# Kernel tuning notes

Measured on AMD Instinct MI355X. Metric: run time of the kernel, lower is better.

## Reference

```python
import jax, jax.numpy as jnp
import numpy as np

EPS = float(np.finfo(np.float64).eps)  # matches np.finfo(float).eps in torch combine()
TOP_K = 2


def setup_inputs() -> dict:
    key = jax.random.key(0)
    k0, k1, k2, k3 = jax.random.split(key, 4)
    N, D, F, E = 8192, 512, 2048, 8
    s = 0.02  # init scale keeps exp() in combine numerically tame
    return {
        "x": jax.random.normal(k0, (N, D), jnp.float32),
        "Wg": jax.random.normal(k1, (D, E), jnp.float32) * s,
        "W1": jax.random.normal(k2, (E, D, F), jnp.float32) * s,
        "b1": jnp.zeros((E, F), jnp.float32),
        "W2": jax.random.normal(k3, (E, F, D), jnp.float32) * s,
        "b2": jnp.zeros((E, D), jnp.float32),
    }


def reference(x, Wg, W1, b1, W2, b2):
    """Sparse-MoE token routing: gate -> dispatch -> per-expert MLP -> combine.

    Faithful to the torch dispatch()/combine() helpers: experts produce
    log-domain outputs; combine() does exp, gate-weighted scatter-add, eps
    floor, then log. Here expressed as dense masked expert compute (zero
    gates annihilate non-routed contributions), which is mathematically
    identical to the gather/index_add formulation and fully vectorized.
    """
    N, D = x.shape
    E = Wg.shape[1]
    # --- gating: noisy-free top-k softmax gates, scattered to [N, E] ---
    logits = x @ Wg                                    # [N, E]
    top_vals, top_idx = jax.lax.top_k(logits, TOP_K)   # [N, K]
    top_gates = jax.nn.softmax(top_vals, axis=-1)      # [N, K]
    gates = jnp.zeros((N, E), x.dtype).at[jnp.arange(N)[:, None], top_idx].set(top_gates)
    # --- expert MLPs (ReLU, per activation='relu' default) ---
    h = jax.nn.relu(jnp.einsum('nd,edf->nef', x, W1) + b1[None])  # [N, E, F]
    o = jnp.einsum('nef,efd->ned', h, W2) + b2[None]              # [N, E, D]
    # --- combine: gate-weighted sum of exp(expert_out), eps floor, log ---
    combined = jnp.einsum('ne,ned->nd', gates, jnp.exp(o))        # [N, D]
    combined = jnp.where(combined == 0, EPS, combined)
    return jnp.log(combined)
```

## Files before the change

### kernel.cpp

```cpp
#include <hip/hip_runtime.h>
#include <stdint.h>
#include <math.h>

#define NTOK 8192
#define DIM  512
#define FDIM 2048
#define NEXP 8
#define RMAX 17408
#define NMT  136
#define KSPLIT 2

typedef __attribute__((ext_vector_type(8))) __bf16 bf16x8;
typedef __attribute__((ext_vector_type(4))) float  f32x4;

#define GTPB 16
#define GB_BLOCKS (NTOK / GTPB)
#define PREP_W1 (GB_BLOCKS)
#define PREP_W2 (GB_BLOCKS + 8192)

#define OFF_W1T    ((size_t)0)
#define SZ_W1T     ((size_t)NEXP * DIM * FDIM * 2)
#define OFF_W2T    (OFF_W1T + SZ_W1T)
#define SZ_W2T     SZ_W1T
#define OFF_H      (OFF_W2T + SZ_W2T)
#define SZ_H       ((size_t)RMAX * FDIM * 2)
#define OFF_META   (OFF_H + SZ_H)
#define SZ_META    ((size_t)1024)
#define OFF_XG     (OFF_META + SZ_META)
#define SZ_XG      ((size_t)RMAX * DIM * 2)
#define OFF_O1     OFF_XG
#define OFF_O0     (OFF_XG + SZ_XG)
#define SZ_O0      ((size_t)RMAX * DIM * 4)
#define OFF_TOKE   (OFF_O0 + SZ_O0)
#define OFF_TOKLS  (OFF_TOKE + (size_t)NTOK * 8)
#define OFF_TOKG   (OFF_TOKLS + (size_t)NTOK * 8)
#define OFF_HISTP  (OFF_TOKG + (size_t)NTOK * 8)
#define OFF_BASEP  (OFF_HISTP + (size_t)GB_BLOCKS * NEXP * 4)
#define OFF_ROWS   (OFF_BASEP + (size_t)GB_BLOCKS * NEXP * 4)

__device__ __forceinline__ unsigned short f2bf(float f) {
  union { float f; unsigned int u; } v; v.f = f;
  unsigned int u = v.u;
  return (unsigned short)((u + 0x7fffu + ((u >> 16) & 1u)) >> 16);
}
__device__ __forceinline__ float bf2f(unsigned short u) {
  union { unsigned int u; float f; } v; v.u = ((unsigned int)u) << 16;
  return v.f;
}

__device__ __forceinline__ void gld16(const unsigned short* g, unsigned short* l) {
  __builtin_amdgcn_global_load_lds(
      (const __attribute__((address_space(1))) void*)g,
      (__attribute__((address_space(3))) void*)l, 16, 0, 0);
}

__device__ __forceinline__ void transpose_tile(const float* __restrict__ src,
                                               unsigned short* __restrict__ dst,
                                               int R, int C, int bx, int by, int bz) {
  __shared__ float t[32][33];
  const int r0 = by * 32, c0 = bx * 32;
  const float* s = src + (size_t)bz * R * C;
  unsigned short* d = dst + (size_t)bz * R * C;
  const int tr = threadIdx.x >> 5, tc = threadIdx.x & 31;
  #pragma unroll
  for (int i = 0; i < 4; i++)
    t[tr + i * 8][tc] = s[(size_t)(r0 + tr + i * 8) * C + (c0 + tc)];
  __syncthreads();
  #pragma unroll
  for (int i = 0; i < 4; i++)
    d[(size_t)(c0 + tr + i * 8) * R + (r0 + tc)] = f2bf(t[tc][tr + i * 8]);
}

__device__ __forceinline__ void gate_body(int gb, const float* __restrict__ x,
                            const float* __restrict__ Wg,
                            int* __restrict__ hist_part, int2* __restrict__ tok_e,
                            int2* __restrict__ tok_ls, float2* __restrict__ tok_g) {
  __shared__ int hist[NEXP];
  __shared__ int le[GTPB][2];
  __shared__ int ls[GTPB][2];
  __shared__ float lg[GTPB][2];
  const int wid = threadIdx.x >> 6;
  const int lane = threadIdx.x & 63;
  if (threadIdx.x < NEXP) hist[threadIdx.x] = 0;
  __syncthreads();
  for (int t = 0; t < 4; t++) {
    const int lt = wid * 4 + t;
    const int n = gb * GTPB + lt;
    double acc[NEXP];
    #pragma unroll
    for (int e = 0; e < NEXP; e++) acc[e] = 0.0;
    #pragma unroll
    for (int i = 0; i < 8; i++) {
      int dd = lane + i * 64;
      double xv = (double)x[(size_t)n * DIM + dd];
      const float* wr = Wg + (size_t)dd * NEXP;
      #pragma unroll
      for (int e = 0; e < NEXP; e++) acc[e] += xv * (double)wr[e];
    }
    #pragma unroll
    for (int s = 32; s > 0; s >>= 1)
      #pragma unroll
      for (int e = 0; e < NEXP; e++) acc[e] += __shfl_xor(acc[e], s, 64);
    if (lane == 0) {
      int i0 = 0;
      #pragma unroll
      for (int e = 1; e < NEXP; e++) if (acc[e] > acc[i0]) i0 = e;
      int i1 = (i0 == 0) ? 1 : 0;
      #pragma unroll
      for (int e = 0; e < NEXP; e++) { if (e == i0 || e == i1) continue; if (acc[e] > acc[i1]) i1 = e; }
      double e1 = exp(acc[i1] - acc[i0]), ssum = 1.0 + e1;
      le[lt][0] = i0; le[lt][1] = i1;
      ls[lt][0] = atomicAdd(&hist[i0], 1);
      ls[lt][1] = atomicAdd(&hist[i1], 1);
      lg[lt][0] = (float)(1.0 / ssum); lg[lt][1] = (float)(e1 / ssum);
    }
  }
  __syncthreads();
  if (threadIdx.x < NEXP) hist_part[gb * NEXP + threadIdx.x] = hist[threadIdx.x];
  if (threadIdx.x < GTPB) {
    const int lt = threadIdx.x;
    const int n = gb * GTPB + lt;
    tok_e[n]  = make_int2(le[lt][0], le[lt][1]);
    tok_ls[n] = make_int2(ls[lt][0], ls[lt][1]);
    tok_g[n]  = make_float2(lg[lt][0], lg[lt][1]);
  }
}

__global__ __launch_bounds__(256) void prep_kernel(const float* __restrict__ W1,
    unsigned short* __restrict__ W1t, const float* __restrict__ W2,
    unsigned short* __restrict__ W2t, const float* __restrict__ x,
    const float* __restrict__ Wg, int* __restrict__ hist_part, int2* __restrict__ tok_e,
    int2* __restrict__ tok_ls, float2* __restrict__ tok_g) {
  const int b = blockIdx.x;
  if (b < GB_BLOCKS) {
    gate_body(b, x, Wg, hist_part, tok_e, tok_ls, tok_g);
  } else if (b < PREP_W2) {
    const int q = b - PREP_W1;
    transpose_tile(W1, W1t, DIM, FDIM, q & 63, (q >> 6) & 15, q >> 10);
  } else {
    const int q = b - PREP_W2;
    transpose_tile(W2, W2t, FDIM, DIM, q & 15, (q >> 4) & 63, q >> 10);
  }
}

__global__ __launch_bounds__(256) void scan_kernel(const int* __restrict__ hist_part,
    int* __restrict__ offsets, int* __restrict__ base_part, int* __restrict__ mtile_e) {
  __shared__ int hp[GB_BLOCKS * NEXP];
  __shared__ int segsum[8][NEXP];
  __shared__ int segbase[8][NEXP];
  __shared__ int tot[NEXP];
  __shared__ int soff[NEXP + 1];
  for (int i = threadIdx.x; i < GB_BLOCKS * NEXP; i += 256) hp[i] = hist_part[i];
  __syncthreads();
  if (threadIdx.x < 64) {
    const int e = threadIdx.x & 7, s = threadIdx.x >> 3;
    int run = 0;
    for (int b = s * 64; b < s * 64 + 64; b++) {
      int v = hp[b * NEXP + e]; hp[b * NEXP + e] = run; run += v;
    }
    segsum[s][e] = run;
  }
  __syncthreads();
  if (threadIdx.x < NEXP) {
    const int e = threadIdx.x;
    int run = 0;
    for (int s = 0; s < 8; s++) { segbase[s][e] = run; run += segsum[s][e]; }
    tot[e] = run;
  }
  __syncthreads();
  if (threadIdx.x == 0) {
    int off = 0;
    for (int e = 0; e < NEXP; e++) { soff[e] = off; offsets[e] = off; off += (tot[e] + 127) & ~127; }
    soff[NEXP] = off; offsets[NEXP] = off;
    for (int t = 0; t < NMT; t++) {
      int r = t * 128, e = NEXP - 1;
      for (int q = 0; q < NEXP; q++)
        if (r >= soff[q] && r < soff[q + 1]) { e = q; break; }
      mtile_e[t] = e;
    }
  }
  __syncthreads();
  for (int i = threadIdx.x; i < GB_BLOCKS * NEXP; i += 256) {
    const int b = i >> 3, e = i & 7;
    base_part[i] = soff[e] + segbase[b >> 6][e] + hp[i];
  }
}

__global__ void gather_kernel(const float* __restrict__ x, const int2* __restrict__ tok_e,
                              const int2* __restrict__ tok_ls, const int* __restrict__ base_part,
                              ushort4* __restrict__ xg, int2* __restrict__ rows) {
  const int n = blockIdx.x;
  int2 te = tok_e[n]; int2 tl = tok_ls[n];
  const int gb = n / GTPB;
  const int r0 = base_part[gb * NEXP + te.x] + tl.x;
  const int r1 = base_part[gb * NEXP + te.y] + tl.y;
  if (threadIdx.x == 0) rows[n] = make_int2(r0, r1);
  const float4* xr = (const float4*)(x + (size_t)n * DIM);
  float4 v = xr[threadIdx.x];
  ushort4 o;
  o.x = f2bf(v.x); o.y = f2bf(v.y); o.z = f2bf(v.z); o.w = f2bf(v.w);
  xg[(size_t)r0 * (DIM / 4) + threadIdx.x] = o;
  xg[(size_t)r1 * (DIM / 4) + threadIdx.x] = o;
}

template <int K, int LDA, int LDB>
__device__ __forceinline__ void gemm_core(const unsigned short* __restrict__ A,
                                          const unsigned short* __restrict__ B,
                                          int m0, int n0, f32x4 acc[4][4]) {
  __shared__ __align__(16) unsigned short As[128 * 64];
  __shared__ __align__(16) unsigned short Bs[128 * 64];
  const int tid = threadIdx.x;
  const int wid = tid >> 6, lane = tid & 63;
  const int wm = (wid >> 1) * 64, wn = (wid & 1) * 64;
  const int quad = lane >> 4, l16 = lane & 15;
  const int srow = tid >> 3;
  const int scol = ((tid & 7) ^ (srow & 7)) << 3;
  unsigned short* As_w = As + 512 * wid;
  unsigned short* Bs_w = Bs + 512 * wid;
  const int r7 = (l16 & 7) << 3;
  const unsigned short* Ar = A + (size_t)(m0 + srow) * LDA + scol;
  const unsigned short* Br = B + (size_t)(n0 + srow) * LDB + scol;
  #pragma unroll 1
  for (int kt = 0; kt < K; kt += 64) {
    __syncthreads();
    #pragma unroll
    for (int p = 0; p < 4; p++) {
      gld16(Ar + (size_t)(32 * p) * LDA + kt, As_w + p * 2048);
      gld16(Br + (size_t)(32 * p) * LDB + kt, Bs_w + p * 2048);
    }
    __syncthreads();
    #pragma unroll
    for (int kk = 0; kk < 2; kk++) {
      const int swz = ((kk * 4 + quad) << 3) ^ r7;
      bf16x8 af[4], bfr[4];
      #pragma unroll
      for (int i = 0; i < 4; i++) {
        af[i]  = *(const bf16x8*)(As + (wm + i * 16 + l16) * 64 + swz);
        bfr[i] = *(const bf16x8*)(Bs + (wn + i * 16 + l16) * 64 + swz);
      }
      #pragma unroll
      for (int mi = 0; mi < 4; mi++)
        #pragma unroll
        for (int ni = 0; ni < 4; ni++)
          acc[mi][ni] = __builtin_amdgcn_mfma_f32_16x16x32_bf16(af[mi], bfr[ni], acc[mi][ni], 0, 0, 0);
    }
  }
}

__global__ __launch_bounds__(256, 4) void gemm1_kernel(const unsigned short* __restrict__ xg,
    const unsigned short* __restrict__ W1t, const int* __restrict__ mtile_e,
    const float* __restrict__ b1, unsigned short* __restrict__ h) {
  const int bm = blockIdx.x, bn = blockIdx.y;
  const int e = mtile_e[bm];
  f32x4 acc[4][4];
  #pragma unroll
  for (int i = 0; i < 4; i++)
    #pragma unroll
    for (int j = 0; j < 4; j++) acc[i][j] = (f32x4){0.f, 0.f, 0.f, 0.f};
  gemm_core<DIM, DIM, DIM>(xg, W1t + (size_t)e * FDIM * DIM, bm * 128, bn * 128, acc);
  const int tid = threadIdx.x, wid = tid >> 6, lane = tid & 63;
  const int wm = (wid >> 1) * 64, wn = (wid & 1) * 64, quad = lane >> 4, l16 = lane & 15;
  #pragma unroll
  for (int mi = 0; mi < 4; mi++) {
    #pragma unroll
    for (int ni = 0; ni < 4; ni++) {
      const int col = bn * 128 + wn + ni * 16 + l16;
      const float bb = b1[e * FDIM + col];
      #pragma unroll
      for (int r = 0; r < 4; r++) {
        const int row = bm * 128 + wm + mi * 16 + quad * 4 + r;
        float v = acc[mi][ni][r] + bb;
        h[(size_t)row * FDIM + col] = f2bf(v > 0.f ? v : 0.f);
      }
    }
  }
}

__global__ __launch_bounds__(256, 4) void gemm2_kernel(const unsigned short* __restrict__ h,
    const unsigned short* __restrict__ W2t, const int* __restrict__ mtile_e,
    float* __restrict__ o0, unsigned short* __restrict__ o1) {
  const int bm = blockIdx.x, bn = blockIdx.y, ks = blockIdx.z;
  const int e = mtile_e[bm];
  const int k0 = ks * (FDIM / KSPLIT);
  f32x4 acc[4][4];
  #pragma unroll
  for (int i = 0; i < 4; i++)
    #pragma unroll
    for (int j = 0; j < 4; j++) acc[i][j] = (f32x4){0.f, 0.f, 0.f, 0.f};
  gemm_core<FDIM / KSPLIT, FDIM, FDIM>(h + k0, W2t + (size_t)e * DIM * FDIM + k0,
                                       bm * 128, bn * 128, acc);
  const int tid = threadIdx.x, wid = tid >> 6, lane = tid & 63;
  const int wm = (wid >> 1) * 64, wn = (wid & 1) * 64, quad = lane >> 4, l16 = lane & 15;
  if (ks == 0) {
    #pragma unroll
    for (int mi = 0; mi < 4; mi++)
      #pragma unroll
      for (int r = 0; r < 4; r++) {
        const int row = bm * 128 + wm + mi * 16 + quad * 4 + r;
        #pragma unroll
        for (int ni = 0; ni < 4; ni++) {
          const int col = bn * 128 + wn + ni * 16 + l16;
          o0[(size_t)row * DIM + col] = acc[mi][ni][r];
        }
      }
  } else {
    #pragma unroll
    for (int mi = 0; mi < 4; mi++)
      #pragma unroll
      for (int r = 0; r < 4; r++) {
        const int row = bm * 128 + wm + mi * 16 + quad * 4 + r;
        #pragma unroll
        for (int ni = 0; ni < 4; ni++) {
          const int col = bn * 128 + wn + ni * 16 + l16;
          o1[(size_t)row * DIM + col] = f2bf(acc[mi][ni][r]);
        }
      }
  }
}

__global__ void combine_kernel(const float* __restrict__ o0, const unsigned short* __restrict__ o1,
                               const int2* __restrict__ tok_e, const int2* __restrict__ rows,
                               const float2* __restrict__ tok_g, const float* __restrict__ b2,
                               float* __restrict__ out) {
  const int n = blockIdx.x;
  const int c = threadIdx.x * 4;
  int2 te = tok_e[n]; int2 rr = rows[n]; float2 tg = tok_g[n];
  const int r0 = rr.x, r1 = rr.y;
  float4 a0 = *(const float4*)(o0 + (size_t)r0 * DIM + c);
  float4 a1 = *(const float4*)(o0 + (size_t)r1 * DIM + c);
  ushort4 p0 = *(const ushort4*)(o1 + (size_t)r0 * DIM + c);
  ushort4 p1 = *(const ushort4*)(o1 + (size_t)r1 * DIM + c);
  float4 c0 = *(const float4*)(b2 + te.x * DIM + c);
  float4 c1 = *(const float4*)(b2 + te.y * DIM + c);
  float4 res;
  #pragma unroll
  for (int j = 0; j < 4; j++) {
    float v0 = ((const float*)&a0)[j] + bf2f(((const unsigned short*)&p0)[j]) + ((const float*)&c0)[j];
    float v1 = ((const float*)&a1)[j] + bf2f(((const unsigned short*)&p1)[j]) + ((const float*)&c1)[j];
    float v = tg.x * expf(v0) + tg.y * expf(v1);
    v = (v == 0.0f) ? 2.220446049250313e-16f : v;
    ((float*)&res)[j] = logf(v);
  }
  *(float4*)(out + (size_t)n * DIM + c) = res;
}

extern "C" void kernel_launch(void* const* d_in, const int* in_sizes, int n_in,
                              void* d_out, int out_size, void* d_ws, size_t ws_size,
                              hipStream_t stream) {
  const float* x  = (const float*)d_in[0];
  const float* Wg = (const float*)d_in[1];
  const float* W1 = (const float*)d_in[2];
  const float* b1 = (const float*)d_in[3];
  const float* W2 = (const float*)d_in[4];
  const float* b2 = (const float*)d_in[5];
  float* out = (float*)d_out;
  char* ws = (char*)d_ws;

  unsigned short* W1t = (unsigned short*)(ws + OFF_W1T);
  unsigned short* W2t = (unsigned short*)(ws + OFF_W2T);
  unsigned short* h   = (unsigned short*)(ws + OFF_H);
  int* meta    = (int*)(ws + OFF_META);
  int* offsets = meta;
  int* mtile_e = meta + 16;
  unsigned short* xg = (unsigned short*)(ws + OFF_XG);
  unsigned short* o1 = (unsigned short*)(ws + OFF_O1);
  float* o0      = (float*)(ws + OFF_O0);
  int2* tok_e    = (int2*)(ws + OFF_TOKE);
  int2* tok_ls   = (int2*)(ws + OFF_TOKLS);
  float2* tok_g  = (float2*)(ws + OFF_TOKG);
  int* hist_part = (int*)(ws + OFF_HISTP);
  int* base_part = (int*)(ws + OFF_BASEP);
  int2* rows     = (int2*)(ws + OFF_ROWS);

  prep_kernel<<<GB_BLOCKS + 2 * 8192, 256, 0, stream>>>(W1, W1t, W2, W2t, x, Wg,
                                                        hist_part, tok_e, tok_ls, tok_g);
  scan_kernel<<<1, 256, 0, stream>>>(hist_part, offsets, base_part, mtile_e);
  gather_kernel<<<NTOK, 128, 0, stream>>>(x, tok_e, tok_ls, base_part, (ushort4*)xg, rows);
  gemm1_kernel<<<dim3(NMT, FDIM / 128), 256, 0, stream>>>(xg, W1t, mtile_e, b1, h);
  gemm2_kernel<<<dim3(NMT, DIM / 128, KSPLIT), 256, 0, stream>>>(h, W2t, mtile_e, o0, o1);
  combine_kernel<<<NTOK, 128, 0, stream>>>(o0, o1, tok_e, rows, tok_g, b2, out);
}
```

Measured before the change: 294.3 us.

## Double-buffer GEMM LDS tiles and use 64x64 weight transpose tiles

The shared GEMM core now keeps two LDS buffers and issues global-to-LDS loads for the next K tile while running MFMAs on the current one, cutting the barrier-separated load/compute stalls to one sync per iteration. Launch bounds drop from 4 to 2 blocks per CU to fit the doubled shared memory. Separately, the weight transpose in the prep kernel moves from 32x32 to 64x64 tiles, launching four times fewer blocks with more work each. The risk is lower occupancy hiding less latency and a larger LDS footprint in the prep kernel.

```diff
diff --git a/kernel.cpp b/kernel.cpp
--- a/kernel.cpp
+++ b/kernel.cpp
@@ -16,7 +16,8 @@
 #define GTPB 16
 #define GB_BLOCKS (NTOK / GTPB)
 #define PREP_W1 (GB_BLOCKS)
-#define PREP_W2 (GB_BLOCKS + 8192)
+#define PREP_W2 (GB_BLOCKS + 2048)
+#define PREP_TOTAL (GB_BLOCKS + 4096)
 
 #define OFF_W1T    ((size_t)0)
 #define SZ_W1T     ((size_t)NEXP * DIM * FDIM * 2)
@@ -54,21 +55,21 @@
       (__attribute__((address_space(3))) void*)l, 16, 0, 0);
 }
 
-__device__ __forceinline__ void transpose_tile(const float* __restrict__ src,
-                                               unsigned short* __restrict__ dst,
-                                               int R, int C, int bx, int by, int bz) {
-  __shared__ float t[32][33];
-  const int r0 = by * 32, c0 = bx * 32;
+__device__ __forceinline__ void transpose_tile64(const float* __restrict__ src,
+                                                 unsigned short* __restrict__ dst,
+                                                 int R, int C, int bx, int by, int bz) {
+  __shared__ float t[64][65];
+  const int r0 = by * 64, c0 = bx * 64;
   const float* s = src + (size_t)bz * R * C;
   unsigned short* d = dst + (size_t)bz * R * C;
-  const int tr = threadIdx.x >> 5, tc = threadIdx.x & 31;
-  #pragma unroll
-  for (int i = 0; i < 4; i++)
-    t[tr + i * 8][tc] = s[(size_t)(r0 + tr + i * 8) * C + (c0 + tc)];
-  __syncthreads();
-  #pragma unroll
-  for (int i = 0; i < 4; i++)
-    d[(size_t)(c0 + tr + i * 8) * R + (r0 + tc)] = f2bf(t[tc][tr + i * 8]);
+  const int tr = threadIdx.x >> 6, tc = threadIdx.x & 63;
+  #pragma unroll
+  for (int i = 0; i < 16; i++)
+    t[tr + i * 4][tc] = s[(size_t)(r0 + tr + i * 4) * C + (c0 + tc)];
+  __syncthreads();
+  #pragma unroll
+  for (int i = 0; i < 16; i++)
+    d[(size_t)(c0 + tr + i * 4) * R + (r0 + tc)] = f2bf(t[tc][tr + i * 4]);
 }
 
 __device__ __forceinline__ void gate_body(int gb, const float* __restrict__ x,
@@ -136,10 +137,10 @@
     gate_body(b, x, Wg, hist_part, tok_e, tok_ls, tok_g);
   } else if (b < PREP_W2) {
     const int q = b - PREP_W1;
-    transpose_tile(W1, W1t, DIM, FDIM, q & 63, (q >> 6) & 15, q >> 10);
+    transpose_tile64(W1, W1t, DIM, FDIM, q & 31, (q >> 5) & 7, q >> 8);
   } else {
     const int q = b - PREP_W2;
-    transpose_tile(W2, W2t, FDIM, DIM, q & 15, (q >> 4) & 63, q >> 10);
+    transpose_tile64(W2, W2t, FDIM, DIM, q & 7, (q >> 3) & 31, q >> 8);
   }
 }
 
@@ -207,36 +208,36 @@
 __device__ __forceinline__ void gemm_core(const unsigned short* __restrict__ A,
                                           const unsigned short* __restrict__ B,
                                           int m0, int n0, f32x4 acc[4][4]) {
-  __shared__ __align__(16) unsigned short As[128 * 64];
-  __shared__ __align__(16) unsigned short Bs[128 * 64];
+  __shared__ __align__(16) unsigned short As[2][128 * 64];
+  __shared__ __align__(16) unsigned short Bs[2][128 * 64];
   const int tid = threadIdx.x;
   const int wid = tid >> 6, lane = tid & 63;
   const int wm = (wid >> 1) * 64, wn = (wid & 1) * 64;
   const int quad = lane >> 4, l16 = lane & 15;
   const int srow = tid >> 3;
   const int scol = ((tid & 7) ^ (srow & 7)) << 3;
-  unsigned short* As_w = As + 512 * wid;
-  unsigned short* Bs_w = Bs + 512 * wid;
   const int r7 = (l16 & 7) << 3;
   const unsigned short* Ar = A + (size_t)(m0 + srow) * LDA + scol;
   const unsigned short* Br = B + (size_t)(n0 + srow) * LDB + scol;
-  #pragma unroll 1
-  for (int kt = 0; kt < K; kt += 64) {
-    __syncthreads();
+
+  auto stage = [&](int c, int kt) {
+    unsigned short* As_w = As[c] + 512 * wid;
+    unsigned short* Bs_w = Bs[c] + 512 * wid;
     #pragma unroll
     for (int p = 0; p < 4; p++) {
       gld16(Ar + (size_t)(32 * p) * LDA + kt, As_w + p * 2048);
       gld16(Br + (size_t)(32 * p) * LDB + kt, Bs_w + p * 2048);
     }
-    __syncthreads();
+  };
+  auto compute = [&](int c) {
     #pragma unroll
     for (int kk = 0; kk < 2; kk++) {
       const int swz = ((kk * 4 + quad) << 3) ^ r7;
       bf16x8 af[4], bfr[4];
       #pragma unroll
       for (int i = 0; i < 4; i++) {
-        af[i]  = *(const bf16x8*)(As + (wm + i * 16 + l16) * 64 + swz);
-        bfr[i] = *(const bf16x8*)(Bs + (wn + i * 16 + l16) * 64 + swz);
+        af[i]  = *(const bf16x8*)(As[c] + (wm + i * 16 + l16) * 64 + swz);
+        bfr[i] = *(const bf16x8*)(Bs[c] + (wn + i * 16 + l16) * 64 + swz);
       }
       #pragma unroll
       for (int mi = 0; mi < 4; mi++)
@@ -244,10 +245,22 @@
         for (int ni = 0; ni < 4; ni++)
           acc[mi][ni] = __builtin_amdgcn_mfma_f32_16x16x32_bf16(af[mi], bfr[ni], acc[mi][ni], 0, 0, 0);
     }
-  }
-}
-
-__global__ __launch_bounds__(256, 4) void gemm1_kernel(const unsigned short* __restrict__ xg,
+  };
+
+  stage(0, 0);
+  __syncthreads();
+  int cur = 0;
+  #pragma unroll 1
+  for (int kt = 64; kt < K; kt += 64) {
+    stage(cur ^ 1, kt);
+    compute(cur);
+    __syncthreads();
+    cur ^= 1;
+  }
+  compute(cur);
+}
+
+__global__ __launch_bounds__(256, 2) void gemm1_kernel(const unsigned short* __restrict__ xg,
     const unsigned short* __restrict__ W1t, const int* __restrict__ mtile_e,
     const float* __restrict__ b1, unsigned short* __restrict__ h) {
   const int bm = blockIdx.x, bn = blockIdx.y;
@@ -276,7 +289,7 @@
   }
 }
 
-__global__ __launch_bounds__(256, 4) void gemm2_kernel(const unsigned short* __restrict__ h,
+__global__ __launch_bounds__(256, 2) void gemm2_kernel(const unsigned short* __restrict__ h,
     const unsigned short* __restrict__ W2t, const int* __restrict__ mtile_e,
     float* __restrict__ o0, unsigned short* __restrict__ o1) {
   const int bm = blockIdx.x, bn = blockIdx.y, ks = blockIdx.z;
@@ -372,8 +385,8 @@
   int* base_part = (int*)(ws + OFF_BASEP);
   int2* rows     = (int2*)(ws + OFF_ROWS);
 
-  prep_kernel<<<GB_BLOCKS + 2 * 8192, 256, 0, stream>>>(W1, W1t, W2, W2t, x, Wg,
-                                                        hist_part, tok_e, tok_ls, tok_g);
+  prep_kernel<<<PREP_TOTAL, 256, 0, stream>>>(W1, W1t, W2, W2t, x, Wg,
+                                              hist_part, tok_e, tok_ls, tok_g);
   scan_kernel<<<1, 256, 0, stream>>>(hist_part, offsets, base_part, mtile_e);
   gather_kernel<<<NTOK, 128, 0, stream>>>(x, tok_e, tok_ls, base_part, (ushort4*)xg, rows);
   gemm1_kernel<<<dim3(NMT, FDIM / 128), 256, 0, stream>>>(xg, W1t, mtile_e, b1, h);
```

New measurement: 295.6 us. About the same (+0.4%).
